# Performance work log

Measured on AMD Instinct MI355X. Metric: run time of the kernel, lower is better.

Reference implementation:

```python
import jax, jax.numpy as jnp
import numpy as np

B, T, C = 8, 1024, 1024   # batch, seq (== block_size), n_embed
H, D = 16, 64             # num_heads, head_size


def setup_inputs() -> dict:
    key = jax.random.key(0)
    kx, kq, kk, kv = jax.random.split(key, 4)
    scale = C ** -0.5  # mimic nn.Linear init scale roughly
    return {
        "x": jax.random.normal(kx, (B, T, C), dtype=jnp.float32),
        "Wq": jax.random.normal(kq, (H, C, D), dtype=jnp.float32) * scale,
        "Wk": jax.random.normal(kk, (H, C, D), dtype=jnp.float32) * scale,
        "Wv": jax.random.normal(kv, (H, C, D), dtype=jnp.float32) * scale,
    }


def reference(x, Wq, Wk, Wv):
    # Per-head Q/K/V projections (batched over heads instead of a Python loop)
    q = jnp.einsum("btc,hcd->bhtd", x, Wq)
    k = jnp.einsum("btc,hcd->bhtd", x, Wk)
    v = jnp.einsum("btc,hcd->bhtd", x, Wv)

    # scaled causal attention scores: [B, H, T, T]
    scores = jnp.einsum("bhtd,bhsd->bhts", q, k) * (D ** -0.5)
    causal = jnp.tril(jnp.ones((T, T), dtype=bool))
    scores = jnp.where(causal, scores, jnp.finfo(scores.dtype).min)
    attn = jax.nn.softmax(scores, axis=-1)

    out = jnp.einsum("bhts,bhsd->bhtd", attn, v)  # [B, H, T, D]
    # concat heads along last dim -> [B, T, H*D]
    return out.transpose(0, 2, 1, 3).reshape(B, T, H * D)
```

## Files before the change

### kernel.cpp

```cpp
#include <hip/hip_runtime.h>
#include <hip/hip_bf16.h>
#include <cstdint>


typedef __attribute__((ext_vector_type(8))) short short8;
typedef __attribute__((ext_vector_type(4))) short bfs4;
typedef __attribute__((ext_vector_type(4))) float f32x4;

__device__ __forceinline__ unsigned short f2bf(float f) {
  union { float f; unsigned int u; } v; v.f = f;
  unsigned int u = v.u;
  return (unsigned short)((u + 0x7fffu + ((u >> 16) & 1u)) >> 16);
}

__device__ __forceinline__ unsigned int pk_bf16(float a, float b) {
  union { __hip_bfloat162 h; unsigned int u; } cv;
  cv.h = __float22bfloat162_rn(make_float2(a, b));
  return cv.u;
}

__device__ __forceinline__ void gload_lds16(const void* g, void* l) {
  __builtin_amdgcn_global_load_lds(
      (const __attribute__((address_space(1))) void*)g,
      (__attribute__((address_space(3))) void*)l, 16, 0, 0);
}

__global__ __launch_bounds__(256) void k_convert_x(const float* __restrict__ x,
                                                   unsigned short* __restrict__ xb) {
  int g = blockIdx.x * 256 + threadIdx.x;
  const float4* xp = (const float4*)x + (size_t)g * 2;
  float4 a = xp[0], b = xp[1];
  short8 o;
  o[0] = (short)f2bf(a.x); o[1] = (short)f2bf(a.y);
  o[2] = (short)f2bf(a.z); o[3] = (short)f2bf(a.w);
  o[4] = (short)f2bf(b.x); o[5] = (short)f2bf(b.y);
  o[6] = (short)f2bf(b.z); o[7] = (short)f2bf(b.w);
  *(short8*)(xb + (size_t)g * 8) = o;
}

__global__ __launch_bounds__(256) void k_convert_w(const float* __restrict__ Wq,
                                                   const float* __restrict__ Wk,
                                                   const float* __restrict__ Wv,
                                                   unsigned short* __restrict__ Wt) {
  int g = blockIdx.x * 256 + threadIdx.x;
  int d  = g & 63;
  int cb = (g >> 6) & 127;
  int h  = (g >> 13) & 15;
  int p  = g >> 17;
  const float* W = (p == 0) ? Wq : (p == 1) ? Wk : Wv;
  const float* src = W + ((size_t)h * 1024 + cb * 8) * 64 + d;
  short8 o;
#pragma unroll
  for (int j = 0; j < 8; ++j) o[j] = (short)f2bf(src[(size_t)j * 64]);
  *(short8*)(Wt + (((size_t)p * 16 + h) * 64 + d) * 1024 + cb * 8) = o;
}

__global__ __launch_bounds__(256) void k_proj(const unsigned short* __restrict__ xb,
                                              const unsigned short* __restrict__ Wt,
                                              unsigned short* __restrict__ Qb,
                                              unsigned short* __restrict__ Kb,
                                              unsigned short* __restrict__ Vt) {
  __shared__ alignas(16) unsigned short As[8192];
  __shared__ alignas(16) unsigned short Bs[8192];
  const int p   = blockIdx.y;
  const int bx  = blockIdx.x;
  const int tid = threadIdx.x;
  const int lane = tid & 63, w = tid >> 6;
  const int ln = lane & 15, quad = lane >> 4;
  const int wm = w >> 1, wn = w & 1;

  const unsigned short* Abase;
  const unsigned short* Bbase;
  int m0, n0;
  const int c = bx & 7, j = bx >> 3;
  if (p < 2) {
    Abase = xb; Bbase = Wt + (size_t)p * 1048576;
    m0 = ((j >> 3) * 8 + c) * 128;
    n0 = (j & 7) * 128;
  } else {
    Abase = Wt + (size_t)2 * 1048576; Bbase = xb;
    n0 = ((j >> 3) * 8 + c) * 128;
    m0 = (j & 7) * 128;
  }

  auto stage = [&](int kt) {
    const int c0 = kt * 64;
#pragma unroll
    for (int i = 0; i < 4; ++i) {
      int idx = i * 256 + tid;
      int iln = idx & 15, iq = (idx >> 4) & 3, imt = (idx >> 6) & 7, ikk = (idx >> 9) & 1;
      int row = imt * 16 + iln;
      int col = c0 + ikk * 32 + iq * 8;
      const int chunk0 = i * 256 + (tid & 192);
      gload_lds16(Abase + (size_t)(m0 + row) * 1024 + col, (char*)As + (size_t)chunk0 * 16);
      gload_lds16(Bbase + (size_t)(n0 + row) * 1024 + col, (char*)Bs + (size_t)chunk0 * 16);
    }
  };

  f32x4 acc[4][4];
#pragma unroll
  for (int i = 0; i < 4; ++i)
#pragma unroll
    for (int jj = 0; jj < 4; ++jj) acc[i][jj] = (f32x4){0.f, 0.f, 0.f, 0.f};

  for (int kt = 0; kt < 16; ++kt) {
    stage(kt);
    __syncthreads();

#pragma unroll
    for (int kk = 0; kk < 2; ++kk) {
      short8 af[4], bfr[4];
#pragma unroll
      for (int t4 = 0; t4 < 4; ++t4) {
        af[t4]  = *(const short8*)&As[(size_t)((((kk * 8 + wm * 4 + t4) * 4 + quad) * 16 + ln)) * 8];
        bfr[t4] = *(const short8*)&Bs[(size_t)((((kk * 8 + wn * 4 + t4) * 4 + quad) * 16 + ln)) * 8];
      }
#pragma unroll
      for (int mt = 0; mt < 4; ++mt)
#pragma unroll
        for (int nt = 0; nt < 4; ++nt)
          acc[mt][nt] = __builtin_amdgcn_mfma_f32_16x16x32_bf16(
              af[mt], bfr[nt], acc[mt][nt], 0, 0, 0);
    }
    __syncthreads();
  }

  unsigned short* outp = (p == 0) ? Qb : (p == 1) ? Kb : Vt;
#pragma unroll
  for (int mt = 0; mt < 4; ++mt)
#pragma unroll
    for (int nt = 0; nt < 4; ++nt)
#pragma unroll
      for (int r = 0; r < 4; ++r) {
        int m = m0 + (wm * 4 + mt) * 16 + quad * 4 + r;
        int n = n0 + (wn * 4 + nt) * 16 + ln;
        size_t addr;
        if (p < 2) {
          addr = ((size_t)(m >> 10) * 16 + (n >> 6)) * 65536 + (size_t)(m & 1023) * 64 + (n & 63);
        } else {
          addr = ((size_t)(n >> 10) * 1024 + m) * 1024 + (n & 1023);
        }
        outp[addr] = f2bf(acc[mt][nt][r]);
      }
}

__global__ __launch_bounds__(256) void k_attn(const unsigned short* __restrict__ Qb,
                                              const unsigned short* __restrict__ Kb,
                                              const unsigned short* __restrict__ Vt,
                                              float* __restrict__ out) {
  __shared__ alignas(16) unsigned short Ks[4096];
  __shared__ alignas(16) unsigned short Vs[4096];
  __shared__ alignas(16) unsigned short Ps[8192];
  const int bid = blockIdx.x;
  const int qb = 7 - (bid >> 7);
  const int bh = bid & 127;
  const int b = bh >> 4, h = bh & 15;
  const int tid = threadIdx.x, lane = tid & 63, w = tid >> 6;
  const int ln = lane & 15, quad = lane >> 4;

  short8 qf[2][2];
#pragma unroll
  for (int qt = 0; qt < 2; ++qt) {
    const int q = qb * 128 + qt * 64 + w * 16 + ln;
#pragma unroll
    for (int kk = 0; kk < 2; ++kk)
      qf[qt][kk] = *(const short8*)(Qb + ((size_t)bh * 1024 + q) * 64 + kk * 32 + quad * 8);
  }

  f32x4 o[2][4];
#pragma unroll
  for (int qt = 0; qt < 2; ++qt)
#pragma unroll
    for (int dt = 0; dt < 4; ++dt) o[qt][dt] = (f32x4){0.f, 0.f, 0.f, 0.f};
  float l_i[2] = {0.f, 0.f};
  const float sc = 0.18033688011112042f;
  const float FM = 16.0f;

  const int ktmax = 2 * qb + 1;

  for (int kt = 0; kt <= ktmax; ++kt) {
    const int s0 = kt * 64;
#pragma unroll
    for (int i = 0; i < 2; ++i) {
      int idx = i * 256 + tid;
      int iln = idx & 15, iq = (idx >> 4) & 3, ikk = (idx >> 6) & 1, it = (idx >> 7) & 3;
      const int chunk0 = i * 256 + (tid & 192);
      gload_lds16(Kb + ((size_t)bh * 1024 + s0 + it * 16 + iln) * 64 + ikk * 32 + iq * 8,
                  (char*)Ks + (size_t)chunk0 * 16);
      gload_lds16(Vt + ((size_t)bh * 64 + it * 16 + iln) * 1024 + s0 + ikk * 32 + iq * 8,
                  (char*)Vs + (size_t)chunk0 * 16);
    }
    __syncthreads();

    f32x4 st[2][4];
#pragma unroll
    for (int s = 0; s < 4; ++s) {
      st[0][s] = (f32x4){0.f, 0.f, 0.f, 0.f};
      st[1][s] = (f32x4){0.f, 0.f, 0.f, 0.f};
#pragma unroll
      for (int kk = 0; kk < 2; ++kk) {
        short8 kf = *(const short8*)&Ks[(size_t)(((s * 2 + kk) * 4 + quad) * 16 + ln) * 8];
        st[0][s] = __builtin_amdgcn_mfma_f32_16x16x32_bf16(kf, qf[0][kk], st[0][s], 0, 0, 0);
        st[1][s] = __builtin_amdgcn_mfma_f32_16x16x32_bf16(kf, qf[1][kk], st[1][s], 0, 0, 0);
      }
    }

#pragma unroll
    for (int qt = 0; qt < 2; ++qt) {
      const int q = qb * 128 + qt * 64 + w * 16 + ln;
      const bool masked = (kt >= 2 * qb + qt);
      float pv[4][4];
      float rs = 0.f;
#pragma unroll
      for (int s = 0; s < 4; ++s)
#pragma unroll
        for (int r = 0; r < 4; ++r) {
          float v = fmaf(st[qt][s][r], sc, -FM);
          if (masked) {
            int sidx = s0 + s * 16 + quad * 4 + r;
            if (sidx > q) v = -1.0e30f;
          }
          float e = __builtin_amdgcn_exp2f(v);
          pv[s][r] = e;
          rs += e;
        }
      rs += __shfl_xor(rs, 16);
      rs += __shfl_xor(rs, 32);
      l_i[qt] += rs;

      unsigned short* Pq = Ps + (w * 2 + qt) * 1024;
#pragma unroll
      for (int s = 0; s < 4; ++s) {
        union { bfs4 v; unsigned int u[2]; } pk;
        pk.u[0] = pk_bf16(pv[s][0], pv[s][1]);
        pk.u[1] = pk_bf16(pv[s][2], pv[s][3]);
        *(bfs4*)&Pq[(s * 2 + (quad >> 1)) * 128 + ln * 8 + (quad & 1) * 4] = pk.v;
      }
    }

#pragma unroll
    for (int kk = 0; kk < 2; ++kk) {
      short8 pf0 = *(const short8*)&Ps[(size_t)(w * 2 + 0) * 1024 + (size_t)((kk * 4 + quad) * 16 + ln) * 8];
      short8 pf1 = *(const short8*)&Ps[(size_t)(w * 2 + 1) * 1024 + (size_t)((kk * 4 + quad) * 16 + ln) * 8];
#pragma unroll
      for (int dt = 0; dt < 4; ++dt) {
        short8 vf = *(const short8*)&Vs[(size_t)(((dt * 2 + kk) * 4 + quad) * 16 + ln) * 8];
        o[0][dt] = __builtin_amdgcn_mfma_f32_16x16x32_bf16(vf, pf0, o[0][dt], 0, 0, 0);
        o[1][dt] = __builtin_amdgcn_mfma_f32_16x16x32_bf16(vf, pf1, o[1][dt], 0, 0, 0);
      }
    }

    __syncthreads();
  }

#pragma unroll
  for (int qt = 0; qt < 2; ++qt) {
    const int q = qb * 128 + qt * 64 + w * 16 + ln;
    const float rl = 1.0f / l_i[qt];
#pragma unroll
    for (int dt = 0; dt < 4; ++dt) {
      float4 ov;
      ov.x = o[qt][dt][0] * rl; ov.y = o[qt][dt][1] * rl;
      ov.z = o[qt][dt][2] * rl; ov.w = o[qt][dt][3] * rl;
      *(float4*)(out + ((size_t)b * 1024 + q) * 1024 + h * 64 + dt * 16 + quad * 4) = ov;
    }
  }
}

extern "C" void kernel_launch(void* const* d_in, const int* in_sizes, int n_in,
                              void* d_out, int out_size, void* d_ws, size_t ws_size,
                              hipStream_t stream) {
  const float* x  = (const float*)d_in[0];
  const float* Wq = (const float*)d_in[1];
  const float* Wk = (const float*)d_in[2];
  const float* Wv = (const float*)d_in[3];
  float* out = (float*)d_out;

  unsigned short* ws = (unsigned short*)d_ws;
  unsigned short* xb = ws;
  unsigned short* Wt = ws + 8388608;
  unsigned short* Qb = ws + 11534336;
  unsigned short* Kb = ws + 19922944;
  unsigned short* Vt = ws + 28311552;

  hipLaunchKernelGGL(k_convert_x, dim3(4096), dim3(256), 0, stream, x, xb);
  hipLaunchKernelGGL(k_convert_w, dim3(1536), dim3(256), 0, stream, Wq, Wk, Wv, Wt);
  hipLaunchKernelGGL(k_proj, dim3(512, 3), dim3(256), 0, stream, xb, Wt, Qb, Kb, Vt);
  hipLaunchKernelGGL(k_attn, dim3(1024), dim3(256), 0, stream, Qb, Kb, Vt, out);
}
```

Baseline: 237.4 us.

## Double-buffer LDS tiles in projection and attention kernels, raise MFMA priority

```diff
diff --git a/kernel.cpp b/kernel.cpp
--- a/kernel.cpp
+++ b/kernel.cpp
@@ -60,8 +60,8 @@
                                               unsigned short* __restrict__ Qb,
                                               unsigned short* __restrict__ Kb,
                                               unsigned short* __restrict__ Vt) {
-  __shared__ alignas(16) unsigned short As[8192];
-  __shared__ alignas(16) unsigned short Bs[8192];
+  __shared__ alignas(16) unsigned short As[2][8192];
+  __shared__ alignas(16) unsigned short Bs[2][8192];
   const int p   = blockIdx.y;
   const int bx  = blockIdx.x;
   const int tid = threadIdx.x;
@@ -83,7 +83,7 @@
     m0 = (j & 7) * 128;
   }
 
-  auto stage = [&](int kt) {
+  auto stage = [&](int kt, int buf) {
     const int c0 = kt * 64;
 #pragma unroll
     for (int i = 0; i < 4; ++i) {
@@ -92,8 +92,8 @@
       int row = imt * 16 + iln;
       int col = c0 + ikk * 32 + iq * 8;
       const int chunk0 = i * 256 + (tid & 192);
-      gload_lds16(Abase + (size_t)(m0 + row) * 1024 + col, (char*)As + (size_t)chunk0 * 16);
-      gload_lds16(Bbase + (size_t)(n0 + row) * 1024 + col, (char*)Bs + (size_t)chunk0 * 16);
+      gload_lds16(Abase + (size_t)(m0 + row) * 1024 + col, (char*)As[buf] + (size_t)chunk0 * 16);
+      gload_lds16(Bbase + (size_t)(n0 + row) * 1024 + col, (char*)Bs[buf] + (size_t)chunk0 * 16);
     }
   };
 
@@ -103,17 +103,22 @@
 #pragma unroll
     for (int jj = 0; jj < 4; ++jj) acc[i][jj] = (f32x4){0.f, 0.f, 0.f, 0.f};
 
+  stage(0, 0);
+  __syncthreads();
+
   for (int kt = 0; kt < 16; ++kt) {
-    stage(kt);
-    __syncthreads();
-
+    const int cur = kt & 1;
+    if (kt < 15) stage(kt + 1, cur ^ 1);
+
+    const unsigned short* Asb = As[cur];
+    const unsigned short* Bsb = Bs[cur];
 #pragma unroll
     for (int kk = 0; kk < 2; ++kk) {
       short8 af[4], bfr[4];
 #pragma unroll
       for (int t4 = 0; t4 < 4; ++t4) {
-        af[t4]  = *(const short8*)&As[(size_t)((((kk * 8 + wm * 4 + t4) * 4 + quad) * 16 + ln)) * 8];
-        bfr[t4] = *(const short8*)&Bs[(size_t)((((kk * 8 + wn * 4 + t4) * 4 + quad) * 16 + ln)) * 8];
+        af[t4]  = *(const short8*)&Asb[(size_t)((((kk * 8 + wm * 4 + t4) * 4 + quad) * 16 + ln)) * 8];
+        bfr[t4] = *(const short8*)&Bsb[(size_t)((((kk * 8 + wn * 4 + t4) * 4 + quad) * 16 + ln)) * 8];
       }
 #pragma unroll
       for (int mt = 0; mt < 4; ++mt)
@@ -148,8 +153,8 @@
                                               const unsigned short* __restrict__ Kb,
                                               const unsigned short* __restrict__ Vt,
                                               float* __restrict__ out) {
-  __shared__ alignas(16) unsigned short Ks[4096];
-  __shared__ alignas(16) unsigned short Vs[4096];
+  __shared__ alignas(16) unsigned short Ks[2][4096];
+  __shared__ alignas(16) unsigned short Vs[2][4096];
   __shared__ alignas(16) unsigned short Ps[8192];
   const int bid = blockIdx.x;
   const int qb = 7 - (bid >> 7);
@@ -158,27 +163,7 @@
   const int tid = threadIdx.x, lane = tid & 63, w = tid >> 6;
   const int ln = lane & 15, quad = lane >> 4;
 
-  short8 qf[2][2];
-#pragma unroll
-  for (int qt = 0; qt < 2; ++qt) {
-    const int q = qb * 128 + qt * 64 + w * 16 + ln;
-#pragma unroll
-    for (int kk = 0; kk < 2; ++kk)
-      qf[qt][kk] = *(const short8*)(Qb + ((size_t)bh * 1024 + q) * 64 + kk * 32 + quad * 8);
-  }
-
-  f32x4 o[2][4];
-#pragma unroll
-  for (int qt = 0; qt < 2; ++qt)
-#pragma unroll
-    for (int dt = 0; dt < 4; ++dt) o[qt][dt] = (f32x4){0.f, 0.f, 0.f, 0.f};
-  float l_i[2] = {0.f, 0.f};
-  const float sc = 0.18033688011112042f;
-  const float FM = 16.0f;
-
-  const int ktmax = 2 * qb + 1;
-
-  for (int kt = 0; kt <= ktmax; ++kt) {
+  auto stage = [&](int kt, int buf) {
     const int s0 = kt * 64;
 #pragma unroll
     for (int i = 0; i < 2; ++i) {
@@ -186,24 +171,57 @@
       int iln = idx & 15, iq = (idx >> 4) & 3, ikk = (idx >> 6) & 1, it = (idx >> 7) & 3;
       const int chunk0 = i * 256 + (tid & 192);
       gload_lds16(Kb + ((size_t)bh * 1024 + s0 + it * 16 + iln) * 64 + ikk * 32 + iq * 8,
-                  (char*)Ks + (size_t)chunk0 * 16);
+                  (char*)Ks[buf] + (size_t)chunk0 * 16);
       gload_lds16(Vt + ((size_t)bh * 64 + it * 16 + iln) * 1024 + s0 + ikk * 32 + iq * 8,
-                  (char*)Vs + (size_t)chunk0 * 16);
-    }
-    __syncthreads();
+                  (char*)Vs[buf] + (size_t)chunk0 * 16);
+    }
+  };
+
+  short8 qf[2][2];
+#pragma unroll
+  for (int qt = 0; qt < 2; ++qt) {
+    const int q = qb * 128 + qt * 64 + w * 16 + ln;
+#pragma unroll
+    for (int kk = 0; kk < 2; ++kk)
+      qf[qt][kk] = *(const short8*)(Qb + ((size_t)bh * 1024 + q) * 64 + kk * 32 + quad * 8);
+  }
+
+  f32x4 o[2][4];
+#pragma unroll
+  for (int qt = 0; qt < 2; ++qt)
+#pragma unroll
+    for (int dt = 0; dt < 4; ++dt) o[qt][dt] = (f32x4){0.f, 0.f, 0.f, 0.f};
+  float l_i[2] = {0.f, 0.f};
+  const float sc = 0.18033688011112042f;
+  const float FM = 16.0f;
+
+  const int ktmax = 2 * qb + 1;
+
+  stage(0, 0);
+  __syncthreads();
+
+  for (int kt = 0; kt <= ktmax; ++kt) {
+    const int cur = kt & 1;
+    const int s0 = kt * 64;
+    if (kt < ktmax) stage(kt + 1, cur ^ 1);
+
+    const unsigned short* Ksb = Ks[cur];
+    const unsigned short* Vsb = Vs[cur];
 
     f32x4 st[2][4];
+    __builtin_amdgcn_s_setprio(1);
 #pragma unroll
     for (int s = 0; s < 4; ++s) {
       st[0][s] = (f32x4){0.f, 0.f, 0.f, 0.f};
       st[1][s] = (f32x4){0.f, 0.f, 0.f, 0.f};
 #pragma unroll
       for (int kk = 0; kk < 2; ++kk) {
-        short8 kf = *(const short8*)&Ks[(size_t)(((s * 2 + kk) * 4 + quad) * 16 + ln) * 8];
+        short8 kf = *(const short8*)&Ksb[(size_t)(((s * 2 + kk) * 4 + quad) * 16 + ln) * 8];
         st[0][s] = __builtin_amdgcn_mfma_f32_16x16x32_bf16(kf, qf[0][kk], st[0][s], 0, 0, 0);
         st[1][s] = __builtin_amdgcn_mfma_f32_16x16x32_bf16(kf, qf[1][kk], st[1][s], 0, 0, 0);
       }
     }
+    __builtin_amdgcn_s_setprio(0);
 
 #pragma unroll
     for (int qt = 0; qt < 2; ++qt) {
@@ -238,17 +256,19 @@
       }
     }
 
+    __builtin_amdgcn_s_setprio(1);
 #pragma unroll
     for (int kk = 0; kk < 2; ++kk) {
       short8 pf0 = *(const short8*)&Ps[(size_t)(w * 2 + 0) * 1024 + (size_t)((kk * 4 + quad) * 16 + ln) * 8];
       short8 pf1 = *(const short8*)&Ps[(size_t)(w * 2 + 1) * 1024 + (size_t)((kk * 4 + quad) * 16 + ln) * 8];
 #pragma unroll
       for (int dt = 0; dt < 4; ++dt) {
-        short8 vf = *(const short8*)&Vs[(size_t)(((dt * 2 + kk) * 4 + quad) * 16 + ln) * 8];
+        short8 vf = *(const short8*)&Vsb[(size_t)(((dt * 2 + kk) * 4 + quad) * 16 + ln) * 8];
         o[0][dt] = __builtin_amdgcn_mfma_f32_16x16x32_bf16(vf, pf0, o[0][dt], 0, 0, 0);
         o[1][dt] = __builtin_amdgcn_mfma_f32_16x16x32_bf16(vf, pf1, o[1][dt], 0, 0, 0);
       }
     }
+    __builtin_amdgcn_s_setprio(0);
 
     __syncthreads();
   }
```

Measured after the change: 260.3 us. +9.6%, slower.
